# Optimization experiments

Hardware: AMD Instinct MI355X
Metric: run time of the kernel (lower is better)

Reference implementation:

```python
import jax, jax.numpy as jnp
import numpy as np
from jax import lax

NY, NU, NHID = 64, 64, 512
NHRZ, NB = 1024, 64


def setup_inputs() -> dict:
    key = jax.random.key(0)
    ks = jax.random.split(key, 9)
    Nh2 = NHID // 2
    r = jax.random.uniform(ks[0], (Nh2,), dtype=jnp.float32)
    theta = jax.random.uniform(ks[1], (Nh2,), dtype=jnp.float32) * (np.pi / 2)
    lmbd_real = r * jnp.cos(theta)
    lmbd_imag = r * jnp.sin(theta)
    B = jax.random.normal(ks[2], (NHID, NU), dtype=jnp.float32) / np.sqrt(NU)
    Wy2x = jax.random.normal(ks[3], (NHID, NY), dtype=jnp.float32) / np.sqrt(NY)
    by2x = jnp.zeros((NHID,), dtype=jnp.float32)
    Wx2y = jax.random.normal(ks[4], (NY, NHID), dtype=jnp.float32) / np.sqrt(NHID)
    bx2y = jnp.zeros((NY,), dtype=jnp.float32)
    y0 = jax.random.normal(ks[5], (NB, NY), dtype=jnp.float32)
    U = jax.random.normal(ks[6], (NHRZ, NB, NU), dtype=jnp.float32)
    return {"y0": y0, "U": U, "lmbd_real": lmbd_real, "lmbd_imag": lmbd_imag,
            "B": B, "Wy2x": Wy2x, "by2x": by2x, "Wx2y": Wx2y, "bx2y": bx2y}


def reference(y0, U, lmbd_real, lmbd_imag, B, Wy2x, by2x, Wx2y, bx2y):
    # Bu[t] = U[t] @ B.T : (Nhrz, NB, NHID)
    Bu = jnp.einsum('tbu,hu->tbh', U, B)
    x0 = y0 @ Wy2x.T + by2x  # (NB, NHID)
    Nh2 = lmbd_real.shape[0]

    # A = [[diag(lr), -diag(li)], [diag(li), diag(lr)]]; x @ A.T == A x per row,
    # which is an elementwise complex (rotation) update on the two halves.
    def step(x, bu):
        x1, x2 = x[:, :Nh2], x[:, Nh2:]
        nx1 = lmbd_real * x1 - lmbd_imag * x2
        nx2 = lmbd_imag * x1 + lmbd_real * x2
        xn = jnp.concatenate([nx1, nx2], axis=-1) + bu
        return xn, xn

    _, X = lax.scan(step, x0, Bu)  # (Nhrz, NB, NHID)
    Y = jnp.einsum('tbh,yh->tby', X, Wx2y) + bx2y
    return Y
```

## Files before the change

### kernel.cpp

```cpp
#include <hip/hip_runtime.h>
#include <hip/hip_bf16.h>
#include <cstddef>
#include <cstdint>

#define NYV 64
#define NUV 64
#define NHID 512
#define NH2 256
#define NTT 1024
#define NBATCH 64
#define CHUNK 64
#define NCHUNK 16
#define XP 520
#define UP 72

typedef __attribute__((ext_vector_type(8))) short bf16x8;
typedef __attribute__((ext_vector_type(4))) float f32x4;
typedef __attribute__((ext_vector_type(8))) short short8v;

__device__ __forceinline__ uint f2bf(float f) {
    union { __hip_bfloat16 h; ushort s; } u;
    u.h = __float2bfloat16(f);
    return (uint)u.s;
}
__device__ __forceinline__ float bf2f_lo(uint d) {
    union { uint u; float f; } v; v.u = d << 16; return v.f;
}
__device__ __forceinline__ float bf2f_hi(uint d) {
    union { uint u; float f; } v; v.u = d & 0xffff0000u; return v.f;
}


template<bool FINAL>
__global__ __launch_bounds__(256) void k_scan(
    const float* __restrict__ U, const float* __restrict__ B,
    const float* __restrict__ lr, const float* __restrict__ li,
    const float* __restrict__ W, const float* __restrict__ bx2y,
    float* __restrict__ carr, float* __restrict__ Y)
{
    __shared__ short Xl[CHUNK * XP];
    __shared__ short Ul[CHUNK * UP];

    const int b  = blockIdx.x;
    const int c  = blockIdx.y;
    const int t0 = c * CHUNK;
    const int tid  = threadIdx.x;
    const int lane = tid & 63;
    const int w    = tid >> 6;
    const int lm   = lane & 15;
    const int lg   = lane >> 4;

    {
        const int t = tid >> 2, q = (tid & 3) * 16;
        const float* up = U + ((size_t)(t0 + t) * NBATCH + b) * NUV + q;
        const float4 f0 = *(const float4*)(up + 0);
        const float4 f1 = *(const float4*)(up + 4);
        const float4 f2 = *(const float4*)(up + 8);
        const float4 f3 = *(const float4*)(up + 12);
        short8v s0, s1;
        s0[0]=(short)f2bf(f0.x); s0[1]=(short)f2bf(f0.y);
        s0[2]=(short)f2bf(f0.z); s0[3]=(short)f2bf(f0.w);
        s0[4]=(short)f2bf(f1.x); s0[5]=(short)f2bf(f1.y);
        s0[6]=(short)f2bf(f1.z); s0[7]=(short)f2bf(f1.w);
        s1[0]=(short)f2bf(f2.x); s1[1]=(short)f2bf(f2.y);
        s1[2]=(short)f2bf(f2.z); s1[3]=(short)f2bf(f2.w);
        s1[4]=(short)f2bf(f3.x); s1[5]=(short)f2bf(f3.y);
        s1[6]=(short)f2bf(f3.z); s1[7]=(short)f2bf(f3.w);
        *(short8v*)&Ul[t*UP + q]     = s0;
        *(short8v*)&Ul[t*UP + q + 8] = s1;
    }
    __syncthreads();

    {
        bf16x8 ufrag[4][2];
        #pragma unroll
        for (int nt = 0; nt < 4; ++nt)
            #pragma unroll
            for (int ks = 0; ks < 2; ++ks)
                ufrag[nt][ks] = *(const bf16x8*)&Ul[(nt*16 + lm)*UP + lg*8 + ks*32];

        #pragma unroll
        for (int i = 0; i < 8; ++i) {
            const int mt = w*8 + i;
            const int hp = mt*16 + lm;
            const int ho = (hp >> 1) + ((hp & 1) << 8);
            bf16x8 a[2];
            #pragma unroll
            for (int ks = 0; ks < 2; ++ks) {
                const float* bp = B + ho*NUV + lg*8 + ks*32;
                const float4 g0 = *(const float4*)(bp);
                const float4 g1 = *(const float4*)(bp + 4);
                bf16x8 t8;
                t8[0]=(short)f2bf(g0.x); t8[1]=(short)f2bf(g0.y);
                t8[2]=(short)f2bf(g0.z); t8[3]=(short)f2bf(g0.w);
                t8[4]=(short)f2bf(g1.x); t8[5]=(short)f2bf(g1.y);
                t8[6]=(short)f2bf(g1.z); t8[7]=(short)f2bf(g1.w);
                a[ks] = t8;
            }
            #pragma unroll
            for (int nt = 0; nt < 4; ++nt) {
                f32x4 acc = {0.f, 0.f, 0.f, 0.f};
                acc = __builtin_amdgcn_mfma_f32_16x16x32_bf16(a[0], ufrag[nt][0], acc, 0, 0, 0);
                acc = __builtin_amdgcn_mfma_f32_16x16x32_bf16(a[1], ufrag[nt][1], acc, 0, 0, 0);
                const int t  = nt*16 + lm;
                const int hb = mt*16 + lg*4;
                uint2 pk;
                pk.x = f2bf(acc[0]) | (f2bf(acc[1]) << 16);
                pk.y = f2bf(acc[2]) | (f2bf(acc[3]) << 16);
                *(uint2*)&Xl[t*XP + hb] = pk;
            }
        }
    }
    __syncthreads();

    {
        const int p = tid;
        const float Lr = lr[p], Li = li[p];
        float x1, x2;
        if (FINAL) {
            const float* cp = carr + ((size_t)c*NBATCH + b)*NHID + 2*p;
            x1 = cp[0]; x2 = cp[1];
        } else { x1 = 0.f; x2 = 0.f; }
        #pragma unroll 8
        for (int t = 0; t < CHUNK; ++t) {
            const uint d = *(const uint*)&Xl[t*XP + 2*p];
            const float n1 = fmaf(Lr, x1, fmaf(-Li, x2, bf2f_lo(d)));
            const float n2 = fmaf(Li, x1, fmaf( Lr, x2, bf2f_hi(d)));
            x1 = n1; x2 = n2;
            if (FINAL) {
                const uint pk = f2bf(x1) | (f2bf(x2) << 16);
                *(uint*)&Xl[t*XP + 2*p] = pk;
            }
        }
        if (!FINAL) {
            float* cp = carr + ((size_t)c*NBATCH + b)*NHID + 2*p;
            cp[0] = x1; cp[1] = x2;
        }
    }

    if constexpr (FINAL) {
        __syncthreads();
        const int y = w*16 + lm;
        const float bias = bx2y[y];
        f32x4 acc[4];
        #pragma unroll
        for (int mt = 0; mt < 4; ++mt) acc[mt] = (f32x4){bias, bias, bias, bias};

        #pragma unroll
        for (int ks = 0; ks < 16; ++ks) {
            const int p0 = lg*4 + ks*16;
            const float4 wr = *(const float4*)(W + (size_t)y*NHID + p0);
            const float4 wi = *(const float4*)(W + (size_t)y*NHID + NH2 + p0);
            bf16x8 bf;
            bf[0]=(short)f2bf(wr.x); bf[1]=(short)f2bf(wi.x);
            bf[2]=(short)f2bf(wr.y); bf[3]=(short)f2bf(wi.y);
            bf[4]=(short)f2bf(wr.z); bf[5]=(short)f2bf(wi.z);
            bf[6]=(short)f2bf(wr.w); bf[7]=(short)f2bf(wi.w);
            const int kb = lg*8 + ks*32;
            #pragma unroll
            for (int mt = 0; mt < 4; ++mt) {
                const bf16x8 xa = *(const bf16x8*)&Xl[(mt*16 + lm)*XP + kb];
                acc[mt] = __builtin_amdgcn_mfma_f32_16x16x32_bf16(xa, bf, acc[mt], 0, 0, 0);
            }
        }
        #pragma unroll
        for (int mt = 0; mt < 4; ++mt) {
            #pragma unroll
            for (int r = 0; r < 4; ++r) {
                const int t = mt*16 + lg*4 + r;
                Y[((size_t)(t0 + t)*NBATCH + b)*NYV + y] = acc[mt][r];
            }
        }
    }
}

__global__ __launch_bounds__(256) void k_carry_prop(
    const float* __restrict__ y0, const float* __restrict__ Wy2x,
    const float* __restrict__ by2x,
    const float* __restrict__ lr, const float* __restrict__ li,
    float* __restrict__ carr)
{
    const int b = blockIdx.x;
    const int p = threadIdx.x;

    float x1 = by2x[p], x2 = by2x[p + NH2];
    #pragma unroll 8
    for (int y = 0; y < NYV; ++y) {
        const float yv = y0[b * NYV + y];
        x1 = fmaf(yv, Wy2x[p * NYV + y], x1);
        x2 = fmaf(yv, Wy2x[(p + NH2) * NYV + y], x2);
    }

    float cr = lr[p], ci = li[p];
    #pragma unroll
    for (int k = 0; k < 6; ++k) {
        const float nr = cr*cr - ci*ci;
        const float ni = 2.f*cr*ci;
        cr = nr; ci = ni;
    }

    for (int c = 0; c < NCHUNK; ++c) {
        float* cp = carr + ((size_t)c*NBATCH + b)*NHID + 2*p;
        const float le1 = cp[0];
        const float le2 = cp[1];
        cp[0] = x1; cp[1] = x2;
        const float n1 = cr*x1 - ci*x2 + le1;
        const float n2 = ci*x1 + cr*x2 + le2;
        x1 = n1; x2 = n2;
    }
}

extern "C" void kernel_launch(void* const* d_in, const int* in_sizes, int n_in,
                              void* d_out, int out_size, void* d_ws, size_t ws_size,
                              hipStream_t stream) {
    const float* y0   = (const float*)d_in[0];
    const float* U    = (const float*)d_in[1];
    const float* lr   = (const float*)d_in[2];
    const float* li   = (const float*)d_in[3];
    const float* B    = (const float*)d_in[4];
    const float* Wy2x = (const float*)d_in[5];
    const float* by2x = (const float*)d_in[6];
    const float* Wx2y = (const float*)d_in[7];
    const float* bx2y = (const float*)d_in[8];
    float* Y    = (float*)d_out;
    float* carr = (float*)d_ws;

    dim3 grid(NBATCH, NCHUNK);
    k_scan<false><<<grid, 256, 0, stream>>>(U, B, lr, li, Wx2y, bx2y, carr, Y);
    k_carry_prop<<<NBATCH, 256, 0, stream>>>(y0, Wy2x, by2x, lr, li, carr);
    k_scan<true ><<<grid, 256, 0, stream>>>(U, B, lr, li, Wx2y, bx2y, carr, Y);
}
```

Measured before the change: 67.53 us.

## Fold carry propagation into the scan kernels and drop the middle launch

Removes the separate carry-propagation kernel. The initial state x0 is now computed by chunk-0 blocks of the first scan pass, and each block of the final pass rebuilds its own incoming carry by replaying the chunk-end states of all earlier chunks. This saves one kernel launch and its serial 16-step chain. In exchange, later chunks do redundant serial work of up to 15 steps with global loads at the start of the final pass.

Result: faster. 65.65 us, median of 6 (-2.8%).

```diff
diff --git a/kernel.cpp b/kernel.cpp
--- a/kernel.cpp
+++ b/kernel.cpp
@@ -7,7 +7,6 @@
 #define NUV 64
 #define NHID 512
 #define NH2 256
-#define NTT 1024
 #define NBATCH 64
 #define CHUNK 64
 #define NCHUNK 16
@@ -36,7 +35,10 @@
     const float* __restrict__ U, const float* __restrict__ B,
     const float* __restrict__ lr, const float* __restrict__ li,
     const float* __restrict__ W, const float* __restrict__ bx2y,
-    float* __restrict__ carr, float* __restrict__ Y)
+    const float* __restrict__ y0, const float* __restrict__ Wy2x,
+    const float* __restrict__ by2x,
+    float* __restrict__ carr, float* __restrict__ x0buf,
+    float* __restrict__ Y)
 {
     __shared__ short Xl[CHUNK * XP];
     __shared__ short Ul[CHUNK * UP];
@@ -118,8 +120,21 @@
         const float Lr = lr[p], Li = li[p];
         float x1, x2;
         if (FINAL) {
-            const float* cp = carr + ((size_t)c*NBATCH + b)*NHID + 2*p;
-            x1 = cp[0]; x2 = cp[1];
+            const float2 x0v = *(const float2*)(x0buf + (size_t)b*NHID + 2*p);
+            x1 = x0v.x; x2 = x0v.y;
+            float cr = Lr, ci = Li;
+            #pragma unroll
+            for (int k = 0; k < 6; ++k) {
+                const float nr = cr*cr - ci*ci;
+                const float ni = 2.f*cr*ci;
+                cr = nr; ci = ni;
+            }
+            for (int cc = 0; cc < c; ++cc) {
+                const float2 le = *(const float2*)(carr + ((size_t)cc*NBATCH + b)*NHID + 2*p);
+                const float n1 = cr*x1 - ci*x2 + le.x;
+                const float n2 = ci*x1 + cr*x2 + le.y;
+                x1 = n1; x2 = n2;
+            }
         } else { x1 = 0.f; x2 = 0.f; }
         #pragma unroll 8
         for (int t = 0; t < CHUNK; ++t) {
@@ -133,8 +148,22 @@
             }
         }
         if (!FINAL) {
-            float* cp = carr + ((size_t)c*NBATCH + b)*NHID + 2*p;
-            cp[0] = x1; cp[1] = x2;
+            float2* cp = (float2*)(carr + ((size_t)c*NBATCH + b)*NHID + 2*p);
+            *cp = make_float2(x1, x2);
+        }
+    }
+
+    if constexpr (!FINAL) {
+        if (c == 0) {
+            const int p = tid;
+            float x1 = by2x[p], x2 = by2x[p + NH2];
+            #pragma unroll 8
+            for (int yv = 0; yv < NYV; ++yv) {
+                const float y0v = y0[b * NYV + yv];
+                x1 = fmaf(y0v, Wy2x[p * NYV + yv], x1);
+                x2 = fmaf(y0v, Wy2x[(p + NH2) * NYV + yv], x2);
+            }
+            *(float2*)(x0buf + (size_t)b * NHID + 2 * p) = make_float2(x1, x2);
         }
     }
 
@@ -142,9 +171,9 @@
         __syncthreads();
         const int y = w*16 + lm;
         const float bias = bx2y[y];
-        f32x4 acc[4];
-        #pragma unroll
-        for (int mt = 0; mt < 4; ++mt) acc[mt] = (f32x4){bias, bias, bias, bias};
+        f32x4 acc2[4];
+        #pragma unroll
+        for (int mt = 0; mt < 4; ++mt) acc2[mt] = (f32x4){bias, bias, bias, bias};
 
         #pragma unroll
         for (int ks = 0; ks < 16; ++ks) {
@@ -160,7 +189,7 @@
             #pragma unroll
             for (int mt = 0; mt < 4; ++mt) {
                 const bf16x8 xa = *(const bf16x8*)&Xl[(mt*16 + lm)*XP + kb];
-                acc[mt] = __builtin_amdgcn_mfma_f32_16x16x32_bf16(xa, bf, acc[mt], 0, 0, 0);
+                acc2[mt] = __builtin_amdgcn_mfma_f32_16x16x32_bf16(xa, bf, acc2[mt], 0, 0, 0);
             }
         }
         #pragma unroll
@@ -168,45 +197,9 @@
             #pragma unroll
             for (int r = 0; r < 4; ++r) {
                 const int t = mt*16 + lg*4 + r;
-                Y[((size_t)(t0 + t)*NBATCH + b)*NYV + y] = acc[mt][r];
-            }
-        }
-    }
-}
-
-__global__ __launch_bounds__(256) void k_carry_prop(
-    const float* __restrict__ y0, const float* __restrict__ Wy2x,
-    const float* __restrict__ by2x,
-    const float* __restrict__ lr, const float* __restrict__ li,
-    float* __restrict__ carr)
-{
-    const int b = blockIdx.x;
-    const int p = threadIdx.x;
-
-    float x1 = by2x[p], x2 = by2x[p + NH2];
-    #pragma unroll 8
-    for (int y = 0; y < NYV; ++y) {
-        const float yv = y0[b * NYV + y];
-        x1 = fmaf(yv, Wy2x[p * NYV + y], x1);
-        x2 = fmaf(yv, Wy2x[(p + NH2) * NYV + y], x2);
-    }
-
-    float cr = lr[p], ci = li[p];
-    #pragma unroll
-    for (int k = 0; k < 6; ++k) {
-        const float nr = cr*cr - ci*ci;
-        const float ni = 2.f*cr*ci;
-        cr = nr; ci = ni;
-    }
-
-    for (int c = 0; c < NCHUNK; ++c) {
-        float* cp = carr + ((size_t)c*NBATCH + b)*NHID + 2*p;
-        const float le1 = cp[0];
-        const float le2 = cp[1];
-        cp[0] = x1; cp[1] = x2;
-        const float n1 = cr*x1 - ci*x2 + le1;
-        const float n2 = ci*x1 + cr*x2 + le2;
-        x1 = n1; x2 = n2;
+                Y[((size_t)(t0 + t)*NBATCH + b)*NYV + y] = acc2[mt][r];
+            }
+        }
     }
 }
 
@@ -223,10 +216,13 @@
     const float* Wx2y = (const float*)d_in[7];
     const float* bx2y = (const float*)d_in[8];
     float* Y    = (float*)d_out;
-    float* carr = (float*)d_ws;
+    char* ws = (char*)d_ws;
+    float* carr  = (float*)(ws);
+    float* x0buf = (float*)(ws + (2u<<20));
 
     dim3 grid(NBATCH, NCHUNK);
-    k_scan<false><<<grid, 256, 0, stream>>>(U, B, lr, li, Wx2y, bx2y, carr, Y);
-    k_carry_prop<<<NBATCH, 256, 0, stream>>>(y0, Wy2x, by2x, lr, li, carr);
-    k_scan<true ><<<grid, 256, 0, stream>>>(U, B, lr, li, Wx2y, bx2y, carr, Y);
-}
+    k_scan<false><<<grid, 256, 0, stream>>>(U, B, lr, li, Wx2y, bx2y,
+                                            y0, Wy2x, by2x, carr, x0buf, Y);
+    k_scan<true ><<<grid, 256, 0, stream>>>(U, B, lr, li, Wx2y, bx2y,
+                                            y0, Wy2x, by2x, carr, x0buf, Y);
+}
```
